# Optimization experiments

Hardware: AMD Instinct MI355X
Metric: run time of the kernel (lower is better)

The kernel has to match this reference:

```python
import jax, jax.numpy as jnp
import numpy as np

N = 50000      # nodes
E = 800000     # edges
IN = 64        # in_channels (also edge_dim)
H = 4          # heads
C = 64         # out_channels per head
SLOPE = 0.2    # PyG GATConv leaky_relu negative_slope
EPS = 1e-16    # PyG softmax eps


def setup_inputs() -> dict:
    key = jax.random.key(0)
    ks = jax.random.split(key, 9)
    s = 1.0 / np.sqrt(IN)
    return {
        "x": jax.random.normal(ks[0], (N, IN), jnp.float32),
        "edge_index": jax.random.randint(ks[1], (2, E), 0, N, jnp.int64),
        "edge_attr": jax.random.normal(ks[2], (E, IN), jnp.float32),
        "W": jax.random.normal(ks[3], (IN, H * C), jnp.float32) * s,
        "W_e": jax.random.normal(ks[4], (IN, H * C), jnp.float32) * s,
        "att_src": jax.random.normal(ks[5], (H, C), jnp.float32) * s,
        "att_dst": jax.random.normal(ks[6], (H, C), jnp.float32) * s,
        "att_edge": jax.random.normal(ks[7], (H, C), jnp.float32) * s,
        "bias": jnp.zeros((H * C,), jnp.float32),
    }


def reference(x, edge_index, edge_attr, W, W_e, att_src, att_dst, att_edge, bias):
    src, dst = edge_index[0], edge_index[1]
    n = x.shape[0]

    # --- add self loops with fill_value='mean' (mean of incoming edge_attr) ---
    deg = jax.ops.segment_sum(jnp.ones((src.shape[0],), x.dtype), dst, num_segments=n)
    loop_attr = jax.ops.segment_sum(edge_attr, dst, num_segments=n) / jnp.maximum(deg, 1.0)[:, None]
    loops = jnp.arange(n, dtype=src.dtype)
    src_f = jnp.concatenate([src, loops])          # [E+N]
    dst_f = jnp.concatenate([dst, loops])          # [E+N]
    ea = jnp.concatenate([edge_attr, loop_attr], axis=0)  # [E+N, IN]

    # --- node / edge projections ---
    h = (x @ W).reshape(n, H, C)                   # [N,H,C]
    a_src = jnp.einsum('nhc,hc->nh', h, att_src)   # [N,H]
    a_dst = jnp.einsum('nhc,hc->nh', h, att_dst)   # [N,H]
    he = (ea @ W_e).reshape(-1, H, C)              # [E+N,H,C]
    a_edge = jnp.einsum('ehc,hc->eh', he, att_edge)

    # --- attention logits + segment softmax over destination nodes ---
    logits = a_src[src_f] + a_dst[dst_f] + a_edge  # [E+N,H]
    logits = jax.nn.leaky_relu(logits, SLOPE)
    m = jax.ops.segment_max(logits, dst_f, num_segments=n)         # every node has a self loop
    e = jnp.exp(logits - m[dst_f])
    z = jax.ops.segment_sum(e, dst_f, num_segments=n)
    alpha = e / (z[dst_f] + EPS)                   # [E+N,H]

    # --- scatter-aggregate messages ---
    msg = h[src_f] * alpha[:, :, None]             # [E+N,H,C]
    out = jax.ops.segment_sum(msg, dst_f, num_segments=n)          # [N,H,C]
    return out.reshape(n, H * C) + bias            # concat heads
```

## Files before the change

### kernel.cpp

```cpp
#include <hip/hip_runtime.h>
#include <hip/hip_bf16.h>
#include <math.h>

#define N_NODES 50000
#define N_EDGES 800000
#define HC      256
#define SLOPE   0.2f

typedef __bf16 bf16x8 __attribute__((ext_vector_type(8)));
typedef float  f32x4  __attribute__((ext_vector_type(4)));

__device__ __forceinline__ unsigned short f2bf(float f) {
    unsigned u = __float_as_uint(f);
    unsigned r = (u + 0x7fffu + ((u >> 16) & 1u)) >> 16;
    return (unsigned short)r;
}

__global__ __launch_bounds__(256) void k_vedge(const float* __restrict__ W_e,
                                               const float* __restrict__ att_edge,
                                               float* __restrict__ v_t) {
    int t = threadIdx.x;
    int k = t >> 2, j = t & 3;
    float s = 0.f;
    #pragma unroll
    for (int c = 0; c < 64; ++c)
        s += W_e[k * HC + j * 64 + c] * att_edge[j * 64 + c];
    v_t[j * 64 + k] = s;
}

__global__ __launch_bounds__(256) void k_proj(const float* __restrict__ x,
                                              const float* __restrict__ W,
                                              const float* __restrict__ att_src,
                                              const float* __restrict__ att_dst,
                                              unsigned short* __restrict__ h_bf,
                                              float* __restrict__ a_src,
                                              float* __restrict__ a_dst) {
    __shared__ unsigned short hs[64 * 256];
    int t = threadIdx.x;
    int lane = t & 63;
    int w = t >> 6;
    int l15 = lane & 15;
    int quad = lane >> 4;
    int row0 = blockIdx.x * 64;

    bf16x8 bh[8], bl[8];
    #pragma unroll
    for (int ct = 0; ct < 4; ++ct) {
        #pragma unroll
        for (int ks = 0; ks < 2; ++ks) {
            bf16x8 h8, l8;
            #pragma unroll
            for (int j = 0; j < 8; ++j) {
                float f = W[(ks * 32 + quad * 8 + j) * 256 + w * 64 + ct * 16 + l15];
                __bf16 hi = (__bf16)f;
                h8[j] = hi;
                l8[j] = (__bf16)(f - (float)hi);
            }
            bh[ct * 2 + ks] = h8;
            bl[ct * 2 + ks] = l8;
        }
    }
    float att_s[4], att_d[4];
    #pragma unroll
    for (int ct = 0; ct < 4; ++ct) {
        att_s[ct] = att_src[w * 64 + ct * 16 + l15];
        att_d[ct] = att_dst[w * 64 + ct * 16 + l15];
    }

    #pragma unroll
    for (int rt = 0; rt < 4; ++rt) {
        int row_a = row0 + rt * 16 + l15;
        if (row_a >= N_NODES) row_a = N_NODES - 1;
        bf16x8 ah[2], al[2];
        #pragma unroll
        for (int ks = 0; ks < 2; ++ks) {
            const float* xp = x + (size_t)row_a * 64 + ks * 32 + quad * 8;
            float4 x0 = ((const float4*)xp)[0];
            float4 x1 = ((const float4*)xp)[1];
            float xf[8] = {x0.x, x0.y, x0.z, x0.w, x1.x, x1.y, x1.z, x1.w};
            bf16x8 h8, l8;
            #pragma unroll
            for (int j = 0; j < 8; ++j) {
                __bf16 hi = (__bf16)xf[j];
                h8[j] = hi;
                l8[j] = (__bf16)(xf[j] - (float)hi);
            }
            ah[ks] = h8;
            al[ks] = l8;
        }
        f32x4 acc[4];
        #pragma unroll
        for (int ct = 0; ct < 4; ++ct) {
            f32x4 a = {0.f, 0.f, 0.f, 0.f};
            a = __builtin_amdgcn_mfma_f32_16x16x32_bf16(ah[0], bh[ct*2+0], a, 0, 0, 0);
            a = __builtin_amdgcn_mfma_f32_16x16x32_bf16(ah[1], bh[ct*2+1], a, 0, 0, 0);
            a = __builtin_amdgcn_mfma_f32_16x16x32_bf16(ah[0], bl[ct*2+0], a, 0, 0, 0);
            a = __builtin_amdgcn_mfma_f32_16x16x32_bf16(ah[1], bl[ct*2+1], a, 0, 0, 0);
            a = __builtin_amdgcn_mfma_f32_16x16x32_bf16(al[0], bh[ct*2+0], a, 0, 0, 0);
            a = __builtin_amdgcn_mfma_f32_16x16x32_bf16(al[1], bh[ct*2+1], a, 0, 0, 0);
            acc[ct] = a;
        }
        #pragma unroll
        for (int ct = 0; ct < 4; ++ct) {
            #pragma unroll
            for (int reg = 0; reg < 4; ++reg) {
                int r = rt * 16 + quad * 4 + reg;
                hs[r * 256 + (ct * 16 + l15) * 4 + w] = f2bf(acc[ct][reg]);
            }
        }
        #pragma unroll
        for (int reg = 0; reg < 4; ++reg) {
            float ps = 0.f, pd = 0.f;
            #pragma unroll
            for (int ct = 0; ct < 4; ++ct) {
                ps += acc[ct][reg] * att_s[ct];
                pd += acc[ct][reg] * att_d[ct];
            }
            #pragma unroll
            for (int off = 1; off < 16; off <<= 1) {
                ps += __shfl_xor(ps, off);
                pd += __shfl_xor(pd, off);
            }
            int row = row0 + rt * 16 + quad * 4 + reg;
            if (l15 == 0 && row < N_NODES) {
                a_src[row * 4 + w] = ps;
                a_dst[row * 4 + w] = pd;
            }
        }
    }
    __syncthreads();
    const uint4* ls = (const uint4*)hs;
    uint4* gd = (uint4*)h_bf;
    #pragma unroll
    for (int i = 0; i < 8; ++i) {
        int g = i * 256 + t;
        int rl = g >> 5;
        if (row0 + rl < N_NODES)
            gd[(size_t)row0 * 32 + g] = ls[g];
    }
}

__global__ __launch_bounds__(256) void k_hist(const int* __restrict__ ei,
                                              int* __restrict__ counts) {
    int e = blockIdx.x * 256 + threadIdx.x;
    if (e < N_EDGES) atomicAdd(&counts[ei[N_EDGES + e]], 1);
}

__global__ __launch_bounds__(1024) void k_scan(const int* __restrict__ cnt,
                                               int* __restrict__ rowptr,
                                               int* __restrict__ cursor) {
    __shared__ int wsum[16];
    int t = threadIdx.x, lane = t & 63, w = t >> 6;
    const int WR = (N_NODES + 15) / 16;
    int begin = w * WR;
    int end = begin + WR; if (end > N_NODES) end = N_NODES;
    int s = 0;
    for (int i = begin + lane; i < end; i += 64) s += cnt[i];
    #pragma unroll
    for (int off = 32; off >= 1; off >>= 1) s += __shfl_xor(s, off);
    if (lane == 0) wsum[w] = s;
    __syncthreads();
    if (t < 16) {
        int orig = wsum[t];
        int v = orig;
        #pragma unroll
        for (int off = 1; off < 16; off <<= 1) {
            int u = __shfl_up(v, off);
            if (t >= off) v += u;
        }
        wsum[t] = v - orig;
    }
    __syncthreads();
    int run = wsum[w];
    int nwin = (end - begin + 63) / 64;
    for (int win = 0; win < nwin; ++win) {
        int i = begin + win * 64 + lane;
        int c = (i < end) ? cnt[i] : 0;
        int v = c;
        #pragma unroll
        for (int off = 1; off < 64; off <<= 1) {
            int u = __shfl_up(v, off);
            if (lane >= off) v += u;
        }
        int excl = run + v - c;
        if (i < end) { rowptr[i] = excl; cursor[i] = excl; }
        run += __shfl(v, 63);
    }
    if (t == 0) rowptr[N_NODES] = N_EDGES;
}

__global__ __launch_bounds__(256) void k_edge(const int* __restrict__ ei,
                                              const float* __restrict__ edge_attr,
                                              const float* __restrict__ v_t,
                                              int* __restrict__ cursor,
                                              float4* __restrict__ edge_ae,
                                              int* __restrict__ sorted_eid) {
    int t = threadIdx.x;
    int lane = t & 63;
    int sub = lane & 15;
    int eq = lane >> 4;
    float4 v0 = ((const float4*)(v_t +   0))[sub];
    float4 v1 = ((const float4*)(v_t +  64))[sub];
    float4 v2 = ((const float4*)(v_t + 128))[sub];
    float4 v3 = ((const float4*)(v_t + 192))[sub];
    int wave_id = blockIdx.x * 4 + (t >> 6);
    int nwaves = gridDim.x * 4;
    const float4* ea4 = (const float4*)edge_attr;
    for (int g = wave_id; g < N_EDGES / 4; g += nwaves) {
        int e = g * 4 + eq;
        float4 ea = ea4[(size_t)e * 16 + sub];
        float p0 = ea.x * v0.x + ea.y * v0.y + ea.z * v0.z + ea.w * v0.w;
        float p1 = ea.x * v1.x + ea.y * v1.y + ea.z * v1.z + ea.w * v1.w;
        float p2 = ea.x * v2.x + ea.y * v2.y + ea.z * v2.z + ea.w * v2.w;
        float p3 = ea.x * v3.x + ea.y * v3.y + ea.z * v3.z + ea.w * v3.w;
        #pragma unroll
        for (int off = 1; off < 16; off <<= 1) {
            p0 += __shfl_xor(p0, off);
            p1 += __shfl_xor(p1, off);
            p2 += __shfl_xor(p2, off);
            p3 += __shfl_xor(p3, off);
        }
        if (sub == 0) {
            int dst = ei[N_EDGES + e];
            int p = atomicAdd(&cursor[dst], 1);
            sorted_eid[p] = e;
            edge_ae[e] = make_float4(p0, p1, p2, p3);
        }
    }
}

__global__ __launch_bounds__(256) void k_gather(const int* __restrict__ rowptr,
                                                const int* __restrict__ sorted_eid,
                                                const float4* __restrict__ edge_ae,
                                                const int* __restrict__ ei,
                                                const unsigned short* __restrict__ h_bf,
                                                const float* __restrict__ a_src,
                                                const float* __restrict__ a_dst,
                                                const float* __restrict__ bias,
                                                float* __restrict__ out) {
    int wave = (int)((blockIdx.x * 256u + threadIdx.x) >> 6);
    int lane = threadIdx.x & 63;
    if (wave >= N_NODES) return;
    int n = wave;
    int r0 = rowptr[n];
    int r1 = rowptr[n + 1];
    float4 ad = ((const float4*)a_dst)[n];
    const uint2* h2 = (const uint2*)h_bf;
    float a0 = 0.f, a1 = 0.f, a2 = 0.f, a3 = 0.f;
    float z0 = 0.f, z1 = 0.f, z2 = 0.f, z3 = 0.f;
    float s0 = 0.f, s1 = 0.f, s2 = 0.f, s3 = 0.f;
    for (int base = r0; base < r1; base += 64) {
        int cnt = r1 - base; if (cnt > 64) cnt = 64;
        int idx = base + (lane < cnt ? lane : 0);
        int eid = sorted_eid[idx];
        float4 ae = edge_ae[eid];
        int msrc = ei[eid];
        float4 asv = ((const float4*)a_src)[msrc];
        float l0 = ae.x + asv.x + ad.x, l1 = ae.y + asv.y + ad.y;
        float l2 = ae.z + asv.z + ad.z, l3 = ae.w + asv.w + ad.w;
        l0 = fmaxf(l0, SLOPE * l0); l1 = fmaxf(l1, SLOPE * l1);
        l2 = fmaxf(l2, SLOPE * l2); l3 = fmaxf(l3, SLOPE * l3);
        float mw0 = __expf(l0), mw1 = __expf(l1);
        float mw2 = __expf(l2), mw3 = __expf(l3);
        if (lane < cnt) {
            z0 += mw0; z1 += mw1; z2 += mw2; z3 += mw3;
            s0 += ae.x; s1 += ae.y; s2 += ae.z; s3 += ae.w;
        }
        #pragma unroll 8
        for (int j = 0; j < cnt; ++j) {
            int src = __shfl(msrc, j);
            float e0 = __shfl(mw0, j), e1 = __shfl(mw1, j);
            float e2 = __shfl(mw2, j), e3 = __shfl(mw3, j);
            uint2 hv = h2[(size_t)src * 64 + lane];
            float h0 = __uint_as_float(hv.x << 16);
            float h1 = __uint_as_float(hv.x & 0xffff0000u);
            float h2f = __uint_as_float(hv.y << 16);
            float h3 = __uint_as_float(hv.y & 0xffff0000u);
            a0 += h0 * e0; a1 += h1 * e1; a2 += h2f * e2; a3 += h3 * e3;
        }
    }
    #pragma unroll
    for (int off = 32; off >= 1; off >>= 1) {
        z0 += __shfl_xor(z0, off); z1 += __shfl_xor(z1, off);
        z2 += __shfl_xor(z2, off); z3 += __shfl_xor(z3, off);
        s0 += __shfl_xor(s0, off); s1 += __shfl_xor(s1, off);
        s2 += __shfl_xor(s2, off); s3 += __shfl_xor(s3, off);
    }
    float d = (float)(r1 - r0); if (d < 1.f) d = 1.f;
    float rdeg = 1.f / d;
    float4 la = ((const float4*)a_src)[n];
    float l0 = la.x + ad.x + s0 * rdeg;
    float l1 = la.y + ad.y + s1 * rdeg;
    float l2 = la.z + ad.z + s2 * rdeg;
    float l3 = la.w + ad.w + s3 * rdeg;
    l0 = fmaxf(l0, SLOPE * l0); l1 = fmaxf(l1, SLOPE * l1);
    l2 = fmaxf(l2, SLOPE * l2); l3 = fmaxf(l3, SLOPE * l3);
    float w0 = __expf(l0), w1 = __expf(l1), w2 = __expf(l2), w3 = __expf(l3);
    uint2 hv = h2[(size_t)n * 64 + lane];
    float h0 = __uint_as_float(hv.x << 16);
    float h1 = __uint_as_float(hv.x & 0xffff0000u);
    float h2f = __uint_as_float(hv.y << 16);
    float h3 = __uint_as_float(hv.y & 0xffff0000u);
    a0 += h0 * w0; z0 += w0;
    a1 += h1 * w1; z1 += w1;
    a2 += h2f * w2; z2 += w2;
    a3 += h3 * w3; z3 += w3;
    size_t ob = (size_t)n * HC + lane;
    out[ob]       = a0 / (z0 + 1e-16f) + bias[lane];
    out[ob + 64]  = a1 / (z1 + 1e-16f) + bias[64 + lane];
    out[ob + 128] = a2 / (z2 + 1e-16f) + bias[128 + lane];
    out[ob + 192] = a3 / (z3 + 1e-16f) + bias[192 + lane];
}

extern "C" void kernel_launch(void* const* d_in, const int* in_sizes, int n_in,
                              void* d_out, int out_size, void* d_ws, size_t ws_size,
                              hipStream_t stream) {
    const float* x        = (const float*)d_in[0];
    const int*   ei       = (const int*)d_in[1];
    const float* edge_attr= (const float*)d_in[2];
    const float* W        = (const float*)d_in[3];
    const float* W_e      = (const float*)d_in[4];
    const float* att_src  = (const float*)d_in[5];
    const float* att_dst  = (const float*)d_in[6];
    const float* att_edge = (const float*)d_in[7];
    const float* bias     = (const float*)d_in[8];
    float* out = (float*)d_out;

    unsigned short* h_bf  = (unsigned short*)d_ws;
    float*  a_src     = (float*)(h_bf + (size_t)N_NODES * 256);
    float*  a_dst     = a_src + N_NODES * 4;
    float*  v_t       = a_dst + N_NODES * 4;
    float4* edge_ae   = (float4*)(v_t + 256);
    int*    sorted_eid= (int*)(edge_ae + N_EDGES);
    int*    rowptr    = sorted_eid + N_EDGES;
    int*    cursor    = rowptr + N_NODES + 1;
    int*    cnt       = cursor + N_NODES;

    hipMemsetAsync(cnt, 0, (size_t)N_NODES * sizeof(int), stream);

    k_vedge<<<1, 256, 0, stream>>>(W_e, att_edge, v_t);
    k_proj<<<(N_NODES + 63) / 64, 256, 0, stream>>>(x, W, att_src, att_dst,
                                                    h_bf, a_src, a_dst);
    k_hist<<<(N_EDGES + 255) / 256, 256, 0, stream>>>(ei, cnt);
    k_scan<<<1, 1024, 0, stream>>>(cnt, rowptr, cursor);
    k_edge<<<2048, 256, 0, stream>>>(ei, edge_attr, v_t, cursor,
                                     edge_ae, sorted_eid);
    k_gather<<<(N_NODES + 3) / 4, 256, 0, stream>>>(rowptr, sorted_eid, edge_ae,
                                                    ei, h_bf, a_src, a_dst,
                                                    bias, out);
}
```

Measured before the change: 511.8 us.

## Fuse vedge and histogram into projection kernel; store edge data in CSR order

Folds the edge-attention vector computation and the destination-degree histogram into the node projection kernel, removing two launches. The edge kernel now writes each edge's source index and attention logits straight to their sorted CSR slot instead of writing an edge-id permutation. The gather kernel can then read them contiguously, dropping two dependent random loads per edge. The scattered writes now move 20 bytes per edge, and the projection kernel does extra atomic work before its main GEMM.

```diff
diff --git a/kernel.cpp b/kernel.cpp
--- a/kernel.cpp
+++ b/kernel.cpp
@@ -16,25 +16,31 @@
     return (unsigned short)r;
 }
 
-__global__ __launch_bounds__(256) void k_vedge(const float* __restrict__ W_e,
-                                               const float* __restrict__ att_edge,
-                                               float* __restrict__ v_t) {
-    int t = threadIdx.x;
-    int k = t >> 2, j = t & 3;
-    float s = 0.f;
-    #pragma unroll
-    for (int c = 0; c < 64; ++c)
-        s += W_e[k * HC + j * 64 + c] * att_edge[j * 64 + c];
-    v_t[j * 64 + k] = s;
-}
-
 __global__ __launch_bounds__(256) void k_proj(const float* __restrict__ x,
                                               const float* __restrict__ W,
                                               const float* __restrict__ att_src,
                                               const float* __restrict__ att_dst,
+                                              const float* __restrict__ W_e,
+                                              const float* __restrict__ att_edge,
+                                              const int* __restrict__ ei,
                                               unsigned short* __restrict__ h_bf,
                                               float* __restrict__ a_src,
-                                              float* __restrict__ a_dst) {
+                                              float* __restrict__ a_dst,
+                                              float* __restrict__ v_t,
+                                              int* __restrict__ counts) {
+    if (blockIdx.x == 0) {
+        int tt = threadIdx.x;
+        int k = tt >> 2, jj = tt & 3;
+        float s = 0.f;
+        #pragma unroll
+        for (int c = 0; c < 64; ++c)
+            s += W_e[k * HC + jj * 64 + c] * att_edge[jj * 64 + c];
+        v_t[jj * 64 + k] = s;
+    }
+    for (int e = blockIdx.x * 256 + threadIdx.x; e < N_EDGES;
+         e += gridDim.x * 256)
+        atomicAdd(&counts[ei[N_EDGES + e]], 1);
+
     __shared__ unsigned short hs[64 * 256];
     int t = threadIdx.x;
     int lane = t & 63;
@@ -138,12 +144,6 @@
         if (row0 + rl < N_NODES)
             gd[(size_t)row0 * 32 + g] = ls[g];
     }
-}
-
-__global__ __launch_bounds__(256) void k_hist(const int* __restrict__ ei,
-                                              int* __restrict__ counts) {
-    int e = blockIdx.x * 256 + threadIdx.x;
-    if (e < N_EDGES) atomicAdd(&counts[ei[N_EDGES + e]], 1);
 }
 
 __global__ __launch_bounds__(1024) void k_scan(const int* __restrict__ cnt,
@@ -193,8 +193,8 @@
                                               const float* __restrict__ edge_attr,
                                               const float* __restrict__ v_t,
                                               int* __restrict__ cursor,
-                                              float4* __restrict__ edge_ae,
-                                              int* __restrict__ sorted_eid) {
+                                              int* __restrict__ ssrc,
+                                              float4* __restrict__ sl4) {
     int t = threadIdx.x;
     int lane = t & 63;
     int sub = lane & 15;
@@ -222,17 +222,17 @@
         }
         if (sub == 0) {
             int dst = ei[N_EDGES + e];
+            int src = ei[e];
             int p = atomicAdd(&cursor[dst], 1);
-            sorted_eid[p] = e;
-            edge_ae[e] = make_float4(p0, p1, p2, p3);
+            ssrc[p] = src;
+            sl4[p] = make_float4(p0, p1, p2, p3);
         }
     }
 }
 
 __global__ __launch_bounds__(256) void k_gather(const int* __restrict__ rowptr,
-                                                const int* __restrict__ sorted_eid,
-                                                const float4* __restrict__ edge_ae,
-                                                const int* __restrict__ ei,
+                                                const int* __restrict__ ssrc,
+                                                const float4* __restrict__ sl4,
                                                 const unsigned short* __restrict__ h_bf,
                                                 const float* __restrict__ a_src,
                                                 const float* __restrict__ a_dst,
@@ -252,9 +252,8 @@
     for (int base = r0; base < r1; base += 64) {
         int cnt = r1 - base; if (cnt > 64) cnt = 64;
         int idx = base + (lane < cnt ? lane : 0);
-        int eid = sorted_eid[idx];
-        float4 ae = edge_ae[eid];
-        int msrc = ei[eid];
+        int msrc = ssrc[idx];
+        float4 ae = sl4[idx];
         float4 asv = ((const float4*)a_src)[msrc];
         float l0 = ae.x + asv.x + ad.x, l1 = ae.y + asv.y + ad.y;
         float l2 = ae.z + asv.z + ad.z, l3 = ae.w + asv.w + ad.w;
@@ -330,22 +329,20 @@
     float*  a_src     = (float*)(h_bf + (size_t)N_NODES * 256);
     float*  a_dst     = a_src + N_NODES * 4;
     float*  v_t       = a_dst + N_NODES * 4;
-    float4* edge_ae   = (float4*)(v_t + 256);
-    int*    sorted_eid= (int*)(edge_ae + N_EDGES);
-    int*    rowptr    = sorted_eid + N_EDGES;
+    float4* sl4       = (float4*)(v_t + 256);
+    int*    ssrc      = (int*)(sl4 + N_EDGES);
+    int*    rowptr    = ssrc + N_EDGES;
     int*    cursor    = rowptr + N_NODES + 1;
     int*    cnt       = cursor + N_NODES;
 
     hipMemsetAsync(cnt, 0, (size_t)N_NODES * sizeof(int), stream);
 
-    k_vedge<<<1, 256, 0, stream>>>(W_e, att_edge, v_t);
     k_proj<<<(N_NODES + 63) / 64, 256, 0, stream>>>(x, W, att_src, att_dst,
-                                                    h_bf, a_src, a_dst);
-    k_hist<<<(N_EDGES + 255) / 256, 256, 0, stream>>>(ei, cnt);
+                                                    W_e, att_edge, ei,
+                                                    h_bf, a_src, a_dst, v_t, cnt);
     k_scan<<<1, 1024, 0, stream>>>(cnt, rowptr, cursor);
-    k_edge<<<2048, 256, 0, stream>>>(ei, edge_attr, v_t, cursor,
-                                     edge_ae, sorted_eid);
-    k_gather<<<(N_NODES + 3) / 4, 256, 0, stream>>>(rowptr, sorted_eid, edge_ae,
-                                                    ei, h_bf, a_src, a_dst,
+    k_edge<<<2048, 256, 0, stream>>>(ei, edge_attr, v_t, cursor, ssrc, sl4);
+    k_gather<<<(N_NODES + 3) / 4, 256, 0, stream>>>(rowptr, ssrc, sl4,
+                                                    h_bf, a_src, a_dst,
                                                     bias, out);
 }
```

New measurement: 500.2 us. -2.3%, faster.
